# Kernel tuning notes

Hardware: AMD Instinct MI355X
Metric: run time of the kernel (lower is better)

Reference implementation:

```python
import jax, jax.numpy as jnp
import numpy as np

DIM_Q = 256
DIM_K = 256
DIM_V = 256
NUM_HEADS = 4


def setup_inputs() -> dict:
    key = jax.random.key(0)
    ks = jax.random.split(key, 12)
    B, NQ, NK = 4, 2048, 2048
    s_in = 1.0 / np.sqrt(DIM_Q)
    s_v = 1.0 / np.sqrt(DIM_V)
    return {
        "Q": jax.random.normal(ks[0], (B, NQ, DIM_Q), jnp.float32),
        "K": jax.random.normal(ks[1], (B, NK, DIM_K), jnp.float32),
        "Wq": jax.random.normal(ks[2], (DIM_V, DIM_Q), jnp.float32) * s_in,
        "bq": jnp.zeros((DIM_V,), jnp.float32),
        "Wk": jax.random.normal(ks[3], (DIM_V, DIM_K), jnp.float32) * s_in,
        "bk": jnp.zeros((DIM_V,), jnp.float32),
        "Wv": jax.random.normal(ks[4], (DIM_V, DIM_K), jnp.float32) * s_in,
        "bv": jnp.zeros((DIM_V,), jnp.float32),
        "Wo": jax.random.normal(ks[5], (DIM_V, DIM_V), jnp.float32) * s_v,
        "bo": jnp.zeros((DIM_V,), jnp.float32),
        "g0": jnp.ones((DIM_V,), jnp.float32),
        "b0": jnp.zeros((DIM_V,), jnp.float32),
        "g1": jnp.ones((DIM_V,), jnp.float32),
        "b1": jnp.zeros((DIM_V,), jnp.float32),
    }


def _layernorm(x, g, b, eps=1e-5):
    mu = jnp.mean(x, axis=-1, keepdims=True)
    var = jnp.mean(jnp.square(x - mu), axis=-1, keepdims=True)
    return (x - mu) * jax.lax.rsqrt(var + eps) * g + b


def _mab(Q, K, Wq, bq, Wk, bk, Wv, bv, Wo, bo, g0, b0, g1, b1):
    B, NQ, _ = Q.shape
    H = NUM_HEADS
    Dh = DIM_V // H  # head dim
    q = jnp.einsum("bqd,ed->bqe", Q, Wq) + bq  # (B,NQ,DV)
    k = jnp.einsum("bkd,ed->bke", K, Wk) + bk
    v = jnp.einsum("bkd,ed->bke", K, Wv) + bv
    # split heads: (B,S,H,Dh) -> (B,H,S,Dh)
    qh = q.reshape(B, NQ, H, Dh).transpose(0, 2, 1, 3)
    kh = k.reshape(B, -1, H, Dh).transpose(0, 2, 1, 3)
    vh = v.reshape(B, -1, H, Dh).transpose(0, 2, 1, 3)
    # NOTE: original scales by sqrt(dim_V), not sqrt(head_dim)
    scores = jnp.einsum("bhqd,bhkd->bhqk", qh, kh) / np.sqrt(DIM_V)
    A = jax.nn.softmax(scores, axis=-1)
    oh = qh + jnp.einsum("bhqk,bhkd->bhqd", A, vh)  # residual with projected Q
    O = oh.transpose(0, 2, 1, 3).reshape(B, NQ, DIM_V)
    O = _layernorm(O, g0, b0)
    O = O + jax.nn.relu(jnp.einsum("bqd,ed->bqe", O, Wo) + bo)
    O = _layernorm(O, g1, b1)
    return O


def reference(Q, K, Wq, bq, Wk, bk, Wv, bv, Wo, bo, g0, b0, g1, b1):
    return _mab(Q, K, Wq, bq, Wk, bk, Wv, bv, Wo, bo, g0, b0, g1, b1)
```

## Files before the change

kernel.cpp:

```cpp
#include <hip/hip_runtime.h>
#include <hip/hip_bf16.h>
#include <math.h>


typedef __attribute__((ext_vector_type(8))) short bf16x8;
typedef __attribute__((ext_vector_type(4))) float f32x4;

static __device__ __forceinline__ unsigned short f2bf(float x) {
  return __bfloat16_as_ushort(__float2bfloat16(x));
}
static __device__ __forceinline__ int pk2(float lo, float hi) {
  return (int)((unsigned)f2bf(lo) | ((unsigned)f2bf(hi) << 16));
}
static __device__ __forceinline__ float exp2_fast(float x) {
  float r; asm("v_exp_f32 %0, %1" : "=v"(r) : "v"(x)); return r;
}

#define SWZ(row, col) ((col) ^ (((row) & 7) << 3))
#define GETC(v,u) ((u)==0?(v).x:((u)==1?(v).y:((u)==2?(v).z:(v).w)))

#define FMA_TILE(a0,a1,a2,a3,b4,u,sacc) do { \
  float a_0=GETC(a0,u), a_1=GETC(a1,u), a_2=GETC(a2,u), a_3=GETC(a3,u); \
  sacc[0][0]=fmaf(a_0,(b4).x,sacc[0][0]); sacc[0][1]=fmaf(a_0,(b4).y,sacc[0][1]); \
  sacc[0][2]=fmaf(a_0,(b4).z,sacc[0][2]); sacc[0][3]=fmaf(a_0,(b4).w,sacc[0][3]); \
  sacc[1][0]=fmaf(a_1,(b4).x,sacc[1][0]); sacc[1][1]=fmaf(a_1,(b4).y,sacc[1][1]); \
  sacc[1][2]=fmaf(a_1,(b4).z,sacc[1][2]); sacc[1][3]=fmaf(a_1,(b4).w,sacc[1][3]); \
  sacc[2][0]=fmaf(a_2,(b4).x,sacc[2][0]); sacc[2][1]=fmaf(a_2,(b4).y,sacc[2][1]); \
  sacc[2][2]=fmaf(a_2,(b4).z,sacc[2][2]); sacc[2][3]=fmaf(a_2,(b4).w,sacc[2][3]); \
  sacc[3][0]=fmaf(a_3,(b4).x,sacc[3][0]); sacc[3][1]=fmaf(a_3,(b4).y,sacc[3][1]); \
  sacc[3][2]=fmaf(a_3,(b4).z,sacc[3][2]); sacc[3][3]=fmaf(a_3,(b4).w,sacc[3][3]); \
} while(0)

__global__ __launch_bounds__(256, 2) void proj_kernel(
    const float* __restrict__ Q, const float* __restrict__ K,
    const float* __restrict__ Wq, const float* __restrict__ bq,
    const float* __restrict__ Wk, const float* __restrict__ bk,
    const float* __restrict__ Wv, const float* __restrict__ bv,
    float* __restrict__ qout, unsigned short* __restrict__ kbf,
    unsigned short* __restrict__ vtb)
{
  __shared__ __align__(16) char smem[18176];
  const int tid = threadIdx.x;
  const int z = blockIdx.z;
  const int bn = blockIdx.x, bm = blockIdx.y;

  if (z == 0) {
    float (*As)[36] = (float(*)[36])smem;
    float (*Wsf)[68] = (float(*)[68])(smem + 9216);
    const int tx = tid & 15, ty = tid >> 4;
    const float* Ablk = Q + (size_t)bm * 64 * 256;
    const float* Wblk = Wq + (size_t)bn * 64 * 256;

    float acc[4][4];
    #pragma unroll
    for (int i = 0; i < 4; ++i)
      #pragma unroll
      for (int j = 0; j < 4; ++j) acc[i][j] = 0.f;

    for (int k0 = 0; k0 < 256; k0 += 32) {
      {
        int idx = tid * 8;
        int r = idx >> 5, c = idx & 31;
        float4 v0 = *(const float4*)(Ablk + (size_t)r * 256 + k0 + c);
        float4 v1 = *(const float4*)(Ablk + (size_t)r * 256 + k0 + c + 4);
        *(float4*)&As[r][c] = v0;
        *(float4*)&As[r][c + 4] = v1;
      }
      {
        int e = tid >> 2, c = (tid & 3) * 8;
        float4 v0 = *(const float4*)(Wblk + (size_t)e * 256 + k0 + c);
        float4 v1 = *(const float4*)(Wblk + (size_t)e * 256 + k0 + c + 4);
        Wsf[c+0][e]=v0.x; Wsf[c+1][e]=v0.y; Wsf[c+2][e]=v0.z; Wsf[c+3][e]=v0.w;
        Wsf[c+4][e]=v1.x; Wsf[c+5][e]=v1.y; Wsf[c+6][e]=v1.z; Wsf[c+7][e]=v1.w;
      }
      __syncthreads();
      #pragma unroll
      for (int kk = 0; kk < 32; kk += 4) {
        float4 a0 = *(const float4*)&As[ty*4+0][kk];
        float4 a1 = *(const float4*)&As[ty*4+1][kk];
        float4 a2 = *(const float4*)&As[ty*4+2][kk];
        float4 a3 = *(const float4*)&As[ty*4+3][kk];
        #pragma unroll
        for (int u = 0; u < 4; ++u) {
          float4 b4 = *(const float4*)&Wsf[kk+u][tx*4];
          FMA_TILE(a0,a1,a2,a3,b4,u,acc);
        }
      }
      __syncthreads();
    }

    const int gm = bm*64 + ty*4, ge = bn*64 + tx*4;
    float4 bv4 = *(const float4*)(bq + ge);
    #pragma unroll
    for (int i = 0; i < 4; ++i) {
      float4 cv;
      cv.x = acc[i][0] + bv4.x; cv.y = acc[i][1] + bv4.y;
      cv.z = acc[i][2] + bv4.z; cv.w = acc[i][3] + bv4.w;
      *(float4*)(qout + (size_t)(gm+i)*256 + ge) = cv;
    }
    return;
  }

  unsigned short (*Ab)[64] = (unsigned short(*)[64])smem;
  unsigned short (*Wb)[64] = (unsigned short(*)[64])(smem + 8192);
  const float* A = K;
  const float* W = (z == 1) ? Wk : Wv;
  const float* bias = (z == 1) ? bk : bv;

  const int wid = tid >> 6, lane = tid & 63;
  const int l15 = lane & 15, g = lane >> 4;
  const int wr = wid >> 1, wc = wid & 1;
  const float* Ablk = A + (size_t)bm * 64 * 256;
  const float* Wblk = W + (size_t)bn * 64 * 256;

  const int sr = tid >> 2, sc = (tid & 3) * 16;
  const int c0 = SWZ(sr, sc), c1 = SWZ(sr, sc + 8);

  f32x4 acc[2][2];
  #pragma unroll
  for (int i = 0; i < 2; ++i)
    #pragma unroll
    for (int j = 0; j < 2; ++j)
      #pragma unroll
      for (int r = 0; r < 4; ++r) acc[i][j][r] = 0.f;

  float4 aR[4], wR[4];
  #pragma unroll
  for (int u = 0; u < 4; ++u) {
    aR[u] = *(const float4*)(Ablk + (size_t)sr*256 + sc + u*4);
    wR[u] = *(const float4*)(Wblk + (size_t)sr*256 + sc + u*4);
  }

  for (int k0 = 0; k0 < 256; k0 += 64) {
    if (k0) __syncthreads();
    int4 pa0 = { pk2(aR[0].x,aR[0].y), pk2(aR[0].z,aR[0].w),
                 pk2(aR[1].x,aR[1].y), pk2(aR[1].z,aR[1].w) };
    int4 pa1 = { pk2(aR[2].x,aR[2].y), pk2(aR[2].z,aR[2].w),
                 pk2(aR[3].x,aR[3].y), pk2(aR[3].z,aR[3].w) };
    int4 pw0 = { pk2(wR[0].x,wR[0].y), pk2(wR[0].z,wR[0].w),
                 pk2(wR[1].x,wR[1].y), pk2(wR[1].z,wR[1].w) };
    int4 pw1 = { pk2(wR[2].x,wR[2].y), pk2(wR[2].z,wR[2].w),
                 pk2(wR[3].x,wR[3].y), pk2(wR[3].z,wR[3].w) };
    *(int4*)&Ab[sr][c0] = pa0;  *(int4*)&Ab[sr][c1] = pa1;
    *(int4*)&Wb[sr][c0] = pw0;  *(int4*)&Wb[sr][c1] = pw1;
    __syncthreads();
    if (k0 < 192) {
      #pragma unroll
      for (int u = 0; u < 4; ++u) {
        aR[u] = *(const float4*)(Ablk + (size_t)sr*256 + (k0+64) + sc + u*4);
        wR[u] = *(const float4*)(Wblk + (size_t)sr*256 + (k0+64) + sc + u*4);
      }
    }
    const unsigned short (*Ta)[64] = (z == 2) ? Wb : Ab;
    const unsigned short (*Tb)[64] = (z == 2) ? Ab : Wb;
    __builtin_amdgcn_s_setprio(1);
    #pragma unroll
    for (int kc = 0; kc < 64; kc += 32) {
      bf16x8 af[2], bf_[2];
      #pragma unroll
      for (int i = 0; i < 2; ++i) {
        int ra = wr*32 + i*16 + l15;
        int rb = wc*32 + i*16 + l15;
        af[i]  = *(const bf16x8*)&Ta[ra][SWZ(ra, kc + g*8)];
        bf_[i] = *(const bf16x8*)&Tb[rb][SWZ(rb, kc + g*8)];
      }
      #pragma unroll
      for (int i = 0; i < 2; ++i)
        #pragma unroll
        for (int j = 0; j < 2; ++j)
          acc[i][j] = __builtin_amdgcn_mfma_f32_16x16x32_bf16(af[i], bf_[j], acc[i][j], 0, 0, 0);
    }
    __builtin_amdgcn_s_setprio(0);
  }

  if (z == 2) {
    const int bvb = bm >> 5;
    const int n0 = (bm & 31) * 64 + wc*32;
    #pragma unroll
    for (int di = 0; di < 2; ++di)
      #pragma unroll
      for (int r = 0; r < 4; ++r) {
        int d = wr*32 + di*16 + g*4 + r;
        float bvs = bias[bn*64 + d];
        #pragma unroll
        for (int ni = 0; ni < 2; ++ni) {
          float c = acc[di][ni][r] + bvs;
          vtb[((size_t)(bvb*4 + bn)*64 + d)*2048 + n0 + ni*16 + l15] = f2bf(c);
        }
      }
    return;
  }

  const int gm = bm*64 + wr*32, ge = bn*64 + wc*32;
  float bv0 = bias[ge + l15], bv1 = bias[ge + 16 + l15];
  #pragma unroll
  for (int mi = 0; mi < 2; ++mi)
    #pragma unroll
    for (int r = 0; r < 4; ++r) {
      int row = gm + mi*16 + g*4 + r;
      #pragma unroll
      for (int ei = 0; ei < 2; ++ei) {
        float c = acc[mi][ei][r] + (ei ? bv1 : bv0);
        kbf[(size_t)row*256 + ge + ei*16 + l15] = f2bf(c);
      }
    }
}

__global__ __launch_bounds__(512, 4) void attn_mfma3(
    const float* __restrict__ q,
    const unsigned short* __restrict__ kb,
    const unsigned short* __restrict__ vt,
    float* __restrict__ o)
{
  __shared__ __align__(16) unsigned short Ks[2][64][64];
  __shared__ __align__(16) unsigned short Vt[2][64][64];
  __shared__ __align__(16) unsigned short Ps[2][64][64];

  const int tid = threadIdx.x;
  const int wid = tid >> 6;
  const int grp = wid >> 2;
  const int w4  = wid & 3;
  const int lane = tid & 63;
  const int l15 = lane & 15;
  const int g = lane >> 4;
  const int lin = blockIdx.x;
  const int xcd = lin & 7, idx = lin >> 3;
  const int bh = xcd * 2 + (idx >> 5);
  const int qb = idx & 31;
  const int b = bh >> 2, h = bh & 3;

  const float qscale = 0.0625f * 1.44269504089f;
  bf16x8 qf[2];
  {
    const float* qp = q + ((size_t)(b*2048 + qb*64 + w4*16 + l15))*256 + h*64;
    #pragma unroll
    for (int ds_ = 0; ds_ < 2; ++ds_) {
      union { bf16x8 v; unsigned short s[8]; } tmp;
      #pragma unroll
      for (int j = 0; j < 8; ++j) tmp.s[j] = f2bf(qp[ds_*32 + g*8 + j] * qscale);
      qf[ds_] = tmp.v;
    }
  }

  const int gt = tid & 255;
  const int sr = gt >> 2, sc = (gt & 3) * 16;
  const int c0 = SWZ(sr, sc), c1 = SWZ(sr, sc + 8);
  const unsigned short* kgp = kb + ((size_t)(b*2048 + grp*1024 + sr))*256 + h*64 + sc;
  const unsigned short* vgp = vt + ((size_t)bh*64 + sr)*2048 + grp*1024 + sc;

  f32x4 oa[4];
  #pragma unroll
  for (int mt = 0; mt < 4; ++mt)
    #pragma unroll
    for (int r = 0; r < 4; ++r) oa[mt][r] = 0.f;
  float m_ = -INFINITY, l_ = 0.f;

  int4 kA0 = *(const int4*)kgp, kA1 = *(const int4*)(kgp + 8);
  int4 vA0 = *(const int4*)vgp, vA1 = *(const int4*)(vgp + 8);

  for (int kt = 0; kt < 16; ++kt) {
    __syncthreads();
    *(int4*)&Ks[grp][sr][c0] = kA0;  *(int4*)&Ks[grp][sr][c1] = kA1;
    *(int4*)&Vt[grp][sr][c0] = vA0;  *(int4*)&Vt[grp][sr][c1] = vA1;
    __syncthreads();
    if (kt < 15) {
      const unsigned short* kn = kgp + (size_t)(kt + 1) * 64 * 256;
      const unsigned short* vn = vgp + (kt + 1) * 64;
      kA0 = *(const int4*)kn;  kA1 = *(const int4*)(kn + 8);
      vA0 = *(const int4*)vn;  vA1 = *(const int4*)(vn + 8);
    }

    f32x4 sa[4];
    #pragma unroll
    for (int mt = 0; mt < 4; ++mt)
      #pragma unroll
      for (int r = 0; r < 4; ++r) sa[mt][r] = 0.f;
    __builtin_amdgcn_s_setprio(1);
    #pragma unroll
    for (int ds_ = 0; ds_ < 2; ++ds_) {
      #pragma unroll
      for (int mt = 0; mt < 4; ++mt) {
        bf16x8 af = *(const bf16x8*)&Ks[grp][mt*16 + l15][SWZ(l15, ds_*32 + g*8)];
        sa[mt] = __builtin_amdgcn_mfma_f32_16x16x32_bf16(af, qf[ds_], sa[mt], 0, 0, 0);
      }
    }
    __builtin_amdgcn_s_setprio(0);

    float mx = sa[0][0];
    #pragma unroll
    for (int mt = 0; mt < 4; ++mt)
      #pragma unroll
      for (int r = 0; r < 4; ++r) mx = fmaxf(mx, sa[mt][r]);
    mx = fmaxf(mx, __shfl_xor(mx, 16, 64));
    mx = fmaxf(mx, __shfl_xor(mx, 32, 64));
    float mn = fmaxf(m_, mx);
    if (__ballot(mx > m_ + 8.f)) {
      float corr = exp2_fast(m_ - mn);
      l_ *= corr;
      #pragma unroll
      for (int mt = 0; mt < 4; ++mt)
        #pragma unroll
        for (int r = 0; r < 4; ++r) oa[mt][r] *= corr;
      m_ = mn;
    }
    float p[16];
    float ps = 0.f;
    #pragma unroll
    for (int mt = 0; mt < 4; ++mt)
      #pragma unroll
      for (int r = 0; r < 4; ++r) {
        float pv = exp2_fast(sa[mt][r] - m_);
        p[mt*4 + r] = pv;
        ps += pv;
      }
    ps += __shfl_xor(ps, 16, 64);
    ps += __shfl_xor(ps, 32, 64);
    l_ += ps;

    #pragma unroll
    for (int mt = 0; mt < 4; ++mt) {
      int2 pv = { pk2(p[mt*4+0], p[mt*4+1]), pk2(p[mt*4+2], p[mt*4+3]) };
      *(int2*)&Ps[grp][w4*16 + l15][SWZ(l15, mt*16 + g*4)] = pv;
    }
    asm volatile("s_waitcnt lgkmcnt(0)" ::: "memory");
    __builtin_amdgcn_sched_barrier(0);

    __builtin_amdgcn_s_setprio(1);
    #pragma unroll
    for (int ks_ = 0; ks_ < 2; ++ks_) {
      bf16x8 pf = *(const bf16x8*)&Ps[grp][w4*16 + l15][SWZ(l15, ks_*32 + g*8)];
      #pragma unroll
      for (int mt = 0; mt < 4; ++mt) {
        bf16x8 vf = *(const bf16x8*)&Vt[grp][mt*16 + l15][SWZ(l15, ks_*32 + g*8)];
        oa[mt] = __builtin_amdgcn_mfma_f32_16x16x32_bf16(vf, pf, oa[mt], 0, 0, 0);
      }
    }
    __builtin_amdgcn_s_setprio(0);
  }

  __syncthreads();
  float* cob = (float*)&Ks[0][0][0];
  float* cml = (float*)&Vt[0][0][0];
  const int ci = w4*64 + lane;
  if (grp == 1) {
    #pragma unroll
    for (int mt = 0; mt < 4; ++mt)
      #pragma unroll
      for (int r = 0; r < 4; ++r) cob[(mt*4 + r)*256 + ci] = oa[mt][r];
    cml[ci] = m_;
    cml[256 + ci] = l_;
  }
  __syncthreads();
  if (grp == 0) {
    float m1 = cml[ci], l1 = cml[256 + ci];
    float mm = fmaxf(m_, m1);
    float cg0 = exp2_fast(m_ - mm), cg1 = exp2_fast(m1 - mm);
    float linv = 1.0f / (l_*cg0 + l1*cg1);
    float* op = o + ((size_t)(b*2048 + qb*64 + w4*16 + l15))*256 + h*64;
    #pragma unroll
    for (int mt = 0; mt < 4; ++mt) {
      int dbase = mt*16 + g*4;
      float4 qv = *(const float4*)(op + dbase);
      float4 st;
      st.x = qv.x + (oa[mt][0]*cg0 + cob[(mt*4+0)*256 + ci]*cg1) * linv;
      st.y = qv.y + (oa[mt][1]*cg0 + cob[(mt*4+1)*256 + ci]*cg1) * linv;
      st.z = qv.z + (oa[mt][2]*cg0 + cob[(mt*4+2)*256 + ci]*cg1) * linv;
      st.w = qv.w + (oa[mt][3]*cg0 + cob[(mt*4+3)*256 + ci]*cg1) * linv;
      *(float4*)(op + dbase) = st;
    }
  }
}

__global__ __launch_bounds__(512) void fused_out(
    const float* __restrict__ x, const float* __restrict__ Wo,
    const float* __restrict__ bo,
    const float* __restrict__ g0v, const float* __restrict__ b0v,
    const float* __restrict__ g1v, const float* __restrict__ b1v,
    float* __restrict__ y)
{
  __shared__ __align__(16) unsigned short As[32][256];
  __shared__ __align__(16) unsigned short Ws[256][64];
  __shared__ float mu_[32], rs_[32];
  float* P = (float*)&Ws[0][0];

  const int tid = threadIdx.x;
  const int w = tid >> 6, lane = tid & 63;
  const int l15 = lane & 15, g = lane >> 4;
  const int r0 = blockIdx.x * 32;

  {
    float4 g4 = *(const float4*)(g0v + lane*4);
    float4 b4 = *(const float4*)(b0v + lane*4);
    #pragma unroll
    for (int rr = 0; rr < 4; ++rr) {
      int m = w*4 + rr;
      const float* xr = x + (size_t)(r0 + m) * 256;
      float4 v = *(const float4*)(xr + lane*4);
      float s = v.x + v.y + v.z + v.w;
      #pragma unroll
      for (int mk = 1; mk <= 32; mk <<= 1) s += __shfl_xor(s, mk, 64);
      float mu = s * (1.0f/256.0f);
      float dx = v.x-mu, dy = v.y-mu, dz = v.z-mu, dw = v.w-mu;
      float qq = dx*dx + dy*dy + dz*dz + dw*dw;
      #pragma unroll
      for (int mk = 1; mk <= 32; mk <<= 1) qq += __shfl_xor(qq, mk, 64);
      float rstd = rsqrtf(qq * (1.0f/256.0f) + 1e-5f);
      if (lane == 0) { mu_[m] = mu; rs_[m] = rstd; }
      float nx = dx*rstd*g4.x + b4.x;
      float ny = dy*rstd*g4.y + b4.y;
      float nz = dz*rstd*g4.z + b4.z;
      float nw = dw*rstd*g4.w + b4.w;
      int2 pv = { pk2(nx, ny), pk2(nz, nw) };
      int col = lane*4;
      *(int2*)&As[m][SWZ(m, col)] = pv;
    }
  }
  __syncthreads();

  const int m0 = (w >> 2) * 16;
  const int e0 = (w & 3) * 64;
  f32x4 acc4[4];
  #pragma unroll
  for (int j = 0; j < 4; ++j)
    #pragma unroll
    for (int r = 0; r < 4; ++r) acc4[j][r] = 0.f;

  for (int k0 = 0; k0 < 256; k0 += 64) {
    if (k0) __syncthreads();
    {
      const int ch = tid & 7;
      const int er = tid >> 3;
      #pragma unroll
      for (int p = 0; p < 4; ++p) {
        int e = p*64 + er;
        const float* wp = Wo + (size_t)e*256 + k0 + ch*8;
        float4 u0 = *(const float4*)wp;
        float4 u1 = *(const float4*)(wp + 4);
        int4 pk = { pk2(u0.x,u0.y), pk2(u0.z,u0.w), pk2(u1.x,u1.y), pk2(u1.z,u1.w) };
        *(int4*)&Ws[e][SWZ(e, ch*8)] = pk;
      }
    }
    __syncthreads();
    __builtin_amdgcn_s_setprio(1);
    #pragma unroll
    for (int ds_ = 0; ds_ < 2; ++ds_) {
      int ma = m0 + l15;
      bf16x8 af = *(const bf16x8*)&As[ma][SWZ(ma, k0 + ds_*32 + g*8)];
      #pragma unroll
      for (int j = 0; j < 4; ++j) {
        int er = e0 + j*16 + l15;
        bf16x8 bfv = *(const bf16x8*)&Ws[er][SWZ(er, ds_*32 + g*8)];
        acc4[j] = __builtin_amdgcn_mfma_f32_16x16x32_bf16(af, bfv, acc4[j], 0, 0, 0);
      }
    }
    __builtin_amdgcn_s_setprio(0);
  }
  __syncthreads();

  #pragma unroll
  for (int j = 0; j < 4; ++j) {
    int e = e0 + j*16 + l15;
    float bov = bo[e], g0e = g0v[e], b0e = b0v[e];
    #pragma unroll
    for (int r = 0; r < 4; ++r) {
      int m = m0 + g*4 + r;
      float xv = x[(size_t)(r0 + m)*256 + e];
      float resv = (xv - mu_[m]) * rs_[m] * g0e + b0e;
      float val = acc4[j][r] + bov;
      P[m*256 + e] = resv + fmaxf(val, 0.f);
    }
  }
  __syncthreads();

  {
    float4 g4 = *(const float4*)(g1v + lane*4);
    float4 b4 = *(const float4*)(b1v + lane*4);
    #pragma unroll
    for (int rr = 0; rr < 4; ++rr) {
      int m = w*4 + rr;
      float4 v = *(const float4*)&P[m*256 + lane*4];
      float s = v.x + v.y + v.z + v.w;
      #pragma unroll
      for (int mk = 1; mk <= 32; mk <<= 1) s += __shfl_xor(s, mk, 64);
      float mu = s * (1.0f/256.0f);
      float dx = v.x-mu, dy = v.y-mu, dz = v.z-mu, dw = v.w-mu;
      float qq = dx*dx + dy*dy + dz*dz + dw*dw;
      #pragma unroll
      for (int mk = 1; mk <= 32; mk <<= 1) qq += __shfl_xor(qq, mk, 64);
      float rstd = rsqrtf(qq * (1.0f/256.0f) + 1e-5f);
      float4 o;
      o.x = dx*rstd*g4.x + b4.x; o.y = dy*rstd*g4.y + b4.y;
      o.z = dz*rstd*g4.z + b4.z; o.w = dw*rstd*g4.w + b4.w;
      *(float4*)(y + (size_t)(r0 + m)*256 + lane*4) = o;
    }
  }
}

extern "C" void kernel_launch(void* const* d_in, const int* in_sizes, int n_in,
                              void* d_out, int out_size, void* d_ws, size_t ws_size,
                              hipStream_t stream) {
  const float* Q  = (const float*)d_in[0];
  const float* K  = (const float*)d_in[1];
  const float* Wq = (const float*)d_in[2];
  const float* bq = (const float*)d_in[3];
  const float* Wk = (const float*)d_in[4];
  const float* bk = (const float*)d_in[5];
  const float* Wv = (const float*)d_in[6];
  const float* bv = (const float*)d_in[7];
  const float* Wo = (const float*)d_in[8];
  const float* bo = (const float*)d_in[9];
  const float* g0 = (const float*)d_in[10];
  const float* b0 = (const float*)d_in[11];
  const float* g1 = (const float*)d_in[12];
  const float* b1 = (const float*)d_in[13];
  float* out = (float*)d_out;

  const size_t SZ = (size_t)4 * 2048 * 256;
  if (ws_size < 2 * SZ * sizeof(unsigned short)) return;

  unsigned short* kbf = (unsigned short*)d_ws;
  unsigned short* vtb = kbf + SZ;

  proj_kernel<<<dim3(4, 128, 3), dim3(256), 0, stream>>>(
      Q, K, Wq, bq, Wk, bk, Wv, bv, out, kbf, vtb);
  attn_mfma3<<<dim3(512), dim3(512), 0, stream>>>(out, kbf, vtb, out);
  fused_out<<<dim3(256), dim3(512), 0, stream>>>(out, Wo, bo, g0, b0, g1, b1, out);
}
```

Before: 81.37 us.

## Double-buffer K/V tiles in attention and use MFMA path for Q projection

The attention kernel now keeps two LDS buffers per group for K and V. The next tile is written into the alternate buffer after compute, and a global prefetch two tiles ahead replaces the two barriers per iteration with one. This needs 80KB of dynamic LDS per block, which may lower occupancy. The Q projection drops the fp32 scalar-FMA path and reuses the bf16 MFMA path, writing fp32 output. That makes the Q projection input rounding coarser.

```diff
diff --git a/kernel.cpp b/kernel.cpp
--- a/kernel.cpp
+++ b/kernel.cpp
@@ -17,19 +17,6 @@
 }
 
 #define SWZ(row, col) ((col) ^ (((row) & 7) << 3))
-#define GETC(v,u) ((u)==0?(v).x:((u)==1?(v).y:((u)==2?(v).z:(v).w)))
-
-#define FMA_TILE(a0,a1,a2,a3,b4,u,sacc) do { \
-  float a_0=GETC(a0,u), a_1=GETC(a1,u), a_2=GETC(a2,u), a_3=GETC(a3,u); \
-  sacc[0][0]=fmaf(a_0,(b4).x,sacc[0][0]); sacc[0][1]=fmaf(a_0,(b4).y,sacc[0][1]); \
-  sacc[0][2]=fmaf(a_0,(b4).z,sacc[0][2]); sacc[0][3]=fmaf(a_0,(b4).w,sacc[0][3]); \
-  sacc[1][0]=fmaf(a_1,(b4).x,sacc[1][0]); sacc[1][1]=fmaf(a_1,(b4).y,sacc[1][1]); \
-  sacc[1][2]=fmaf(a_1,(b4).z,sacc[1][2]); sacc[1][3]=fmaf(a_1,(b4).w,sacc[1][3]); \
-  sacc[2][0]=fmaf(a_2,(b4).x,sacc[2][0]); sacc[2][1]=fmaf(a_2,(b4).y,sacc[2][1]); \
-  sacc[2][2]=fmaf(a_2,(b4).z,sacc[2][2]); sacc[2][3]=fmaf(a_2,(b4).w,sacc[2][3]); \
-  sacc[3][0]=fmaf(a_3,(b4).x,sacc[3][0]); sacc[3][1]=fmaf(a_3,(b4).y,sacc[3][1]); \
-  sacc[3][2]=fmaf(a_3,(b4).z,sacc[3][2]); sacc[3][3]=fmaf(a_3,(b4).w,sacc[3][3]); \
-} while(0)
 
 __global__ __launch_bounds__(256, 2) void proj_kernel(
     const float* __restrict__ Q, const float* __restrict__ K,
@@ -39,73 +26,15 @@
     float* __restrict__ qout, unsigned short* __restrict__ kbf,
     unsigned short* __restrict__ vtb)
 {
-  __shared__ __align__(16) char smem[18176];
+  __shared__ __align__(16) unsigned short Ab[64][64];
+  __shared__ __align__(16) unsigned short Wb[64][64];
   const int tid = threadIdx.x;
   const int z = blockIdx.z;
   const int bn = blockIdx.x, bm = blockIdx.y;
 
-  if (z == 0) {
-    float (*As)[36] = (float(*)[36])smem;
-    float (*Wsf)[68] = (float(*)[68])(smem + 9216);
-    const int tx = tid & 15, ty = tid >> 4;
-    const float* Ablk = Q + (size_t)bm * 64 * 256;
-    const float* Wblk = Wq + (size_t)bn * 64 * 256;
-
-    float acc[4][4];
-    #pragma unroll
-    for (int i = 0; i < 4; ++i)
-      #pragma unroll
-      for (int j = 0; j < 4; ++j) acc[i][j] = 0.f;
-
-    for (int k0 = 0; k0 < 256; k0 += 32) {
-      {
-        int idx = tid * 8;
-        int r = idx >> 5, c = idx & 31;
-        float4 v0 = *(const float4*)(Ablk + (size_t)r * 256 + k0 + c);
-        float4 v1 = *(const float4*)(Ablk + (size_t)r * 256 + k0 + c + 4);
-        *(float4*)&As[r][c] = v0;
-        *(float4*)&As[r][c + 4] = v1;
-      }
-      {
-        int e = tid >> 2, c = (tid & 3) * 8;
-        float4 v0 = *(const float4*)(Wblk + (size_t)e * 256 + k0 + c);
-        float4 v1 = *(const float4*)(Wblk + (size_t)e * 256 + k0 + c + 4);
-        Wsf[c+0][e]=v0.x; Wsf[c+1][e]=v0.y; Wsf[c+2][e]=v0.z; Wsf[c+3][e]=v0.w;
-        Wsf[c+4][e]=v1.x; Wsf[c+5][e]=v1.y; Wsf[c+6][e]=v1.z; Wsf[c+7][e]=v1.w;
-      }
-      __syncthreads();
-      #pragma unroll
-      for (int kk = 0; kk < 32; kk += 4) {
-        float4 a0 = *(const float4*)&As[ty*4+0][kk];
-        float4 a1 = *(const float4*)&As[ty*4+1][kk];
-        float4 a2 = *(const float4*)&As[ty*4+2][kk];
-        float4 a3 = *(const float4*)&As[ty*4+3][kk];
-        #pragma unroll
-        for (int u = 0; u < 4; ++u) {
-          float4 b4 = *(const float4*)&Wsf[kk+u][tx*4];
-          FMA_TILE(a0,a1,a2,a3,b4,u,acc);
-        }
-      }
-      __syncthreads();
-    }
-
-    const int gm = bm*64 + ty*4, ge = bn*64 + tx*4;
-    float4 bv4 = *(const float4*)(bq + ge);
-    #pragma unroll
-    for (int i = 0; i < 4; ++i) {
-      float4 cv;
-      cv.x = acc[i][0] + bv4.x; cv.y = acc[i][1] + bv4.y;
-      cv.z = acc[i][2] + bv4.z; cv.w = acc[i][3] + bv4.w;
-      *(float4*)(qout + (size_t)(gm+i)*256 + ge) = cv;
-    }
-    return;
-  }
-
-  unsigned short (*Ab)[64] = (unsigned short(*)[64])smem;
-  unsigned short (*Wb)[64] = (unsigned short(*)[64])(smem + 8192);
-  const float* A = K;
-  const float* W = (z == 1) ? Wk : Wv;
-  const float* bias = (z == 1) ? bk : bv;
+  const float* A    = (z == 0) ? Q  : K;
+  const float* W    = (z == 0) ? Wq : ((z == 1) ? Wk : Wv);
+  const float* bias = (z == 0) ? bq : ((z == 1) ? bk : bv);
 
   const int wid = tid >> 6, lane = tid & 63;
   const int l15 = lane & 15, g = lane >> 4;
@@ -201,20 +130,24 @@
       #pragma unroll
       for (int ei = 0; ei < 2; ++ei) {
         float c = acc[mi][ei][r] + (ei ? bv1 : bv0);
-        kbf[(size_t)row*256 + ge + ei*16 + l15] = f2bf(c);
-      }
-    }
-}
-
-__global__ __launch_bounds__(512, 4) void attn_mfma3(
+        if (z == 0) qout[(size_t)row*256 + ge + ei*16 + l15] = c;
+        else        kbf [(size_t)row*256 + ge + ei*16 + l15] = f2bf(c);
+      }
+    }
+}
+
+typedef unsigned short tile64_t[64][64];
+
+__global__ __launch_bounds__(512, 4) void attn_mfma4(
     const float* __restrict__ q,
     const unsigned short* __restrict__ kb,
     const unsigned short* __restrict__ vt,
     float* __restrict__ o)
 {
-  __shared__ __align__(16) unsigned short Ks[2][64][64];
-  __shared__ __align__(16) unsigned short Vt[2][64][64];
-  __shared__ __align__(16) unsigned short Ps[2][64][64];
+  extern __shared__ __align__(16) char smem_dyn[];
+  tile64_t* Ks = (tile64_t*)smem_dyn;
+  tile64_t* Vt = (tile64_t*)(smem_dyn + 32768);
+  tile64_t* Ps = (tile64_t*)(smem_dyn + 65536);
 
   const int tid = threadIdx.x;
   const int wid = tid >> 6;
@@ -255,20 +188,22 @@
     for (int r = 0; r < 4; ++r) oa[mt][r] = 0.f;
   float m_ = -INFINITY, l_ = 0.f;
 
-  int4 kA0 = *(const int4*)kgp, kA1 = *(const int4*)(kgp + 8);
-  int4 vA0 = *(const int4*)vgp, vA1 = *(const int4*)(vgp + 8);
+  {
+    int4 k0_ = *(const int4*)kgp, k1_ = *(const int4*)(kgp + 8);
+    int4 v0_ = *(const int4*)vgp, v1_ = *(const int4*)(vgp + 8);
+    *(int4*)&Ks[grp*2+0][sr][c0] = k0_;  *(int4*)&Ks[grp*2+0][sr][c1] = k1_;
+    *(int4*)&Vt[grp*2+0][sr][c0] = v0_;  *(int4*)&Vt[grp*2+0][sr][c1] = v1_;
+  }
+  int4 kA0 = *(const int4*)(kgp + (size_t)64*256);
+  int4 kA1 = *(const int4*)(kgp + (size_t)64*256 + 8);
+  int4 vA0 = *(const int4*)(vgp + 64);
+  int4 vA1 = *(const int4*)(vgp + 64 + 8);
+  __syncthreads();
 
   for (int kt = 0; kt < 16; ++kt) {
-    __syncthreads();
-    *(int4*)&Ks[grp][sr][c0] = kA0;  *(int4*)&Ks[grp][sr][c1] = kA1;
-    *(int4*)&Vt[grp][sr][c0] = vA0;  *(int4*)&Vt[grp][sr][c1] = vA1;
-    __syncthreads();
-    if (kt < 15) {
-      const unsigned short* kn = kgp + (size_t)(kt + 1) * 64 * 256;
-      const unsigned short* vn = vgp + (kt + 1) * 64;
-      kA0 = *(const int4*)kn;  kA1 = *(const int4*)(kn + 8);
-      vA0 = *(const int4*)vn;  vA1 = *(const int4*)(vn + 8);
-    }
+    const int cur = kt & 1;
+    const tile64_t& Kc = Ks[grp*2 + cur];
+    const tile64_t& Vc = Vt[grp*2 + cur];
 
     f32x4 sa[4];
     #pragma unroll
@@ -280,7 +215,7 @@
     for (int ds_ = 0; ds_ < 2; ++ds_) {
       #pragma unroll
       for (int mt = 0; mt < 4; ++mt) {
-        bf16x8 af = *(const bf16x8*)&Ks[grp][mt*16 + l15][SWZ(l15, ds_*32 + g*8)];
+        bf16x8 af = *(const bf16x8*)&Kc[mt*16 + l15][SWZ(l15, ds_*32 + g*8)];
         sa[mt] = __builtin_amdgcn_mfma_f32_16x16x32_bf16(af, qf[ds_], sa[mt], 0, 0, 0);
       }
     }
@@ -331,16 +266,29 @@
       bf16x8 pf = *(const bf16x8*)&Ps[grp][w4*16 + l15][SWZ(l15, ks_*32 + g*8)];
       #pragma unroll
       for (int mt = 0; mt < 4; ++mt) {
-        bf16x8 vf = *(const bf16x8*)&Vt[grp][mt*16 + l15][SWZ(l15, ks_*32 + g*8)];
+        bf16x8 vf = *(const bf16x8*)&Vc[mt*16 + l15][SWZ(l15, ks_*32 + g*8)];
         oa[mt] = __builtin_amdgcn_mfma_f32_16x16x32_bf16(vf, pf, oa[mt], 0, 0, 0);
       }
     }
     __builtin_amdgcn_s_setprio(0);
-  }
-
-  __syncthreads();
-  float* cob = (float*)&Ks[0][0][0];
-  float* cml = (float*)&Vt[0][0][0];
+
+    if (kt < 15) {
+      *(int4*)&Ks[grp*2+(cur^1)][sr][c0] = kA0;
+      *(int4*)&Ks[grp*2+(cur^1)][sr][c1] = kA1;
+      *(int4*)&Vt[grp*2+(cur^1)][sr][c0] = vA0;
+      *(int4*)&Vt[grp*2+(cur^1)][sr][c1] = vA1;
+      if (kt < 14) {
+        const unsigned short* kn = kgp + (size_t)(kt + 2) * 64 * 256;
+        const unsigned short* vn = vgp + (kt + 2) * 64;
+        kA0 = *(const int4*)kn;  kA1 = *(const int4*)(kn + 8);
+        vA0 = *(const int4*)vn;  vA1 = *(const int4*)(vn + 8);
+      }
+    }
+    __syncthreads();
+  }
+
+  float* cob = (float*)smem_dyn;
+  float* cml = (float*)(smem_dyn + 32768);
   const int ci = w4*64 + lane;
   if (grp == 1) {
     #pragma unroll
@@ -521,8 +469,12 @@
   unsigned short* kbf = (unsigned short*)d_ws;
   unsigned short* vtb = kbf + SZ;
 
+  const int ATTN_LDS = 81920;
+  hipFuncSetAttribute((const void*)attn_mfma4,
+                      hipFuncAttributeMaxDynamicSharedMemorySize, ATTN_LDS);
+
   proj_kernel<<<dim3(4, 128, 3), dim3(256), 0, stream>>>(
       Q, K, Wq, bq, Wk, bk, Wv, bv, out, kbf, vtb);
-  attn_mfma3<<<dim3(512), dim3(512), 0, stream>>>(out, kbf, vtb, out);
+  attn_mfma4<<<dim3(512), dim3(512), ATTN_LDS, stream>>>(out, kbf, vtb, out);
   fused_out<<<dim3(256), dim3(512), 0, stream>>>(out, Wo, bo, g0, b0, g1, b1, out);
 }
```

New measurement: 74.13 us. 1.1x faster.
